# Performance work log

Measured on AMD Instinct MI355X. Metric: run time of the kernel, lower is better.

## Reference

```python
import jax, jax.numpy as jnp
import numpy as np

B, L, N, D = 32, 48, 325, 128


def setup_inputs() -> dict:
    key = jax.random.key(0)
    k1, k2, k3, k4, k5 = jax.random.split(key, 5)
    s = 1.0 / np.sqrt(D)  # PyTorch GRUCell init scale
    return {
        "X": jax.random.normal(k1, (B, L, N, D), dtype=jnp.float32),
        "W_ih": jax.random.uniform(k2, (3 * D, D), jnp.float32, -s, s),
        "W_hh": jax.random.uniform(k3, (3 * D, D), jnp.float32, -s, s),
        "b_ih": jax.random.uniform(k4, (3 * D,), jnp.float32, -s, s),
        "b_hh": jax.random.uniform(k5, (3 * D,), jnp.float32, -s, s),
    }


def reference(X, W_ih, W_hh, b_ih, b_hh):
    # X: (B, L, N, D) -> (B*N, L, D), matching X.transpose(1,2).reshape(B*N, L, D)
    b, l, n, d = X.shape
    x = jnp.transpose(X, (0, 2, 1, 3)).reshape(b * n, l, d)
    # Precompute all input-side gate projections once: (BN, L, 3D)
    gi = jnp.einsum("tlf,gf->tlg", x, W_ih) + b_ih
    gi_t = jnp.swapaxes(gi, 0, 1)  # (L, BN, 3D) for scan over time

    def step(h, gi_step):
        gh = h @ W_hh.T + b_hh  # (BN, 3D)
        i_r, i_z, i_n = jnp.split(gi_step, 3, axis=-1)
        h_r, h_z, h_n = jnp.split(gh, 3, axis=-1)
        r = jax.nn.sigmoid(i_r + h_r)
        z = jax.nn.sigmoid(i_z + h_z)
        ng = jnp.tanh(i_n + r * h_n)
        h_new = (1.0 - z) * ng + z * h
        return h_new, h_new

    h0 = jnp.zeros((b * n, d), dtype=X.dtype)
    _, outs = jax.lax.scan(step, h0, gi_t)
    # Dropout is identity in eval mode; original stacks along dim 0 -> (L, B*N, D)
    return outs
```

## Files before the change

kernel.cpp:

```cpp
#include <hip/hip_runtime.h>
#include <hip/hip_bf16.h>
#include <stdint.h>


constexpr int Bdim = 32;
constexpr int Ldim = 48;
constexpr int Nseq = 325;
constexpr int Ddim = 128;
constexpr int BN   = Bdim * Nseq;
constexpr int MT   = 48;
constexpr int NBLK = (BN + MT - 1) / MT;
constexpr int RS   = 136;
constexpr int XR32 = 528;
constexpr int XR16 = 272;
constexpr int HBUF_B = 2 * MT * RS * 2;
constexpr int SMEM_B = HBUF_B + 2 * MT * XR32;

typedef __bf16 bf16;
typedef __bf16 bf16x4 __attribute__((ext_vector_type(4)));
typedef __bf16 bf16x8 __attribute__((ext_vector_type(8)));
typedef float  floatx4 __attribute__((ext_vector_type(4)));
typedef float  floatx8 __attribute__((ext_vector_type(8)));

__device__ __forceinline__ float fast_sigmoid(float x) {
    return __builtin_amdgcn_rcpf(1.f + __expf(-x));
}
__device__ __forceinline__ float fast_tanh(float x) {
    const float e = __expf(-2.f * __builtin_fabsf(x));
    const float t = (1.f - e) * __builtin_amdgcn_rcpf(1.f + e);
    return __builtin_copysignf(t, x);
}

__device__ __forceinline__ bool detect_f32(const void* wih) {
    const bf16* p = (const bf16*)wih;
    bool f32 = false;
#pragma unroll
    for (int i = 0; i < 128; i += 2) {
        const float v = __builtin_fabsf((float)p[i]);
        if (!(v <= 0.125f)) f32 = true;
    }
    return f32;
}

template <bool F32>
__device__ __forceinline__ bf16x8 load8(const void* base, size_t off) {
    if constexpr (F32) {
        const floatx8 v = *(const floatx8*)((const float*)base + off);
        return __builtin_convertvector(v, bf16x8);
    } else {
        return *(const bf16x8*)((const bf16*)base + off);
    }
}
template <bool F32>
__device__ __forceinline__ float lds1(const void* base, int i) {
    if constexpr (F32) return ((const float*)base)[i];
    else               return (float)((const bf16*)base)[i];
}

__device__ __forceinline__ void gload_lds4(const void* g, void* l) {
    __builtin_amdgcn_global_load_lds(
        (const __attribute__((address_space(1))) void*)g,
        (__attribute__((address_space(3))) void*)l, 4, 0, 0);
}

template <bool F32>
__device__ __forceinline__ bf16x8 xfrag(const char* xb, int row, int kbase) {
    if constexpr (F32) {
        const float* p = (const float*)(xb + row * XR32) + kbase;
        const floatx4 a = *(const floatx4*)p;
        const floatx4 b = *(const floatx4*)(p + 4);
        const bf16x4 lo = __builtin_convertvector(a, bf16x4);
        const bf16x4 hi = __builtin_convertvector(b, bf16x4);
        return __builtin_shufflevector(lo, hi, 0, 1, 2, 3, 4, 5, 6, 7);
    } else {
        return *(const bf16x8*)((const bf16*)(xb + row * XR16) + kbase);
    }
}

template <bool F32>
__device__ __forceinline__ void gru_body(
    const void* __restrict__ X, const void* __restrict__ Wih,
    const void* __restrict__ Whh, const void* __restrict__ bih,
    const void* __restrict__ bhh, void* __restrict__ out,
    char* __restrict__ smem)
{
    const int tid  = threadIdx.x;
    const int wave = tid >> 6;
    const int lane = tid & 63;
    const int l16  = lane & 15;
    const int q    = lane >> 4;
    const int t0   = blockIdx.x * MT;
    const int dcol = wave * 16 + l16;

    bf16* hbuf = (bf16*)smem;
    char* xbuf = smem + HBUF_B;
    constexpr int XROWB   = F32 ? XR32 : XR16;
    constexpr int XBUF_B  = MT * XROWB;
    constexpr uint32_t lstride = (uint32_t)Nseq * Ddim * (F32 ? 4u : 2u);

    bf16x8 wih_f[3][4], whh_f[3][4];
#pragma unroll
    for (int g = 0; g < 3; ++g) {
        const size_t rowoffw = (size_t)(g * 128 + dcol) * Ddim + q * 8;
#pragma unroll
        for (int kk = 0; kk < 4; ++kk) {
            wih_f[g][kk] = load8<F32>(Wih, rowoffw + kk * 32);
            whh_f[g][kk] = load8<F32>(Whh, rowoffw + kk * 32);
        }
    }

    const float bias_r  = lds1<F32>(bih, dcol)       + lds1<F32>(bhh, dcol);
    const float bias_z  = lds1<F32>(bih, 128 + dcol) + lds1<F32>(bhh, 128 + dcol);
    const float bias_in = lds1<F32>(bih, 256 + dcol);
    const float bias_hn = lds1<F32>(bhh, 256 + dcol);

    const int srow0 = wave * 6;
    const char* Xc = (const char*)X;
    uint32_t rowoff[6];
#pragma unroll
    for (int i = 0; i < 6; ++i) {
        int t = t0 + srow0 + i;
        if (t >= BN) t = BN - 1;
        const int b = t / Nseq;
        const int n = t - b * Nseq;
        rowoff[i] = (((uint32_t)b * (Ldim * Nseq) + (uint32_t)n) * Ddim) * (F32 ? 4u : 2u)
                  + ((uint32_t)lane << 2);
    }

    auto stage = [&](char* xb, uint32_t loff) {
#pragma unroll
        for (int i = 0; i < 6; ++i) {
            const char* g = Xc + rowoff[i] + loff;
            char* d = xb + (srow0 + i) * XROWB;
            gload_lds4(g, d);
            if constexpr (F32) gload_lds4(g + 256, d + 256);
        }
    };

    for (int i = tid; i < MT * RS; i += 512) hbuf[i] = (bf16)0.f;
    stage(xbuf, 0);
    floatx4 hreg[3];
#pragma unroll
    for (int mt = 0; mt < 3; ++mt) hreg[mt] = floatx4{0.f, 0.f, 0.f, 0.f};
    __syncthreads();

    int cur = 0;
    for (int l = 0; l < Ldim; ++l) {
        const char* xc = xbuf + cur * XBUF_B;
        const bf16* hc = hbuf + cur * (MT * RS);

        bf16x8 xf[3][4];
#pragma unroll
        for (int mt = 0; mt < 3; ++mt)
#pragma unroll
            for (int kk = 0; kk < 4; ++kk)
                xf[mt][kk] = xfrag<F32>(xc, mt * 16 + l16, kk * 32 + q * 8);

        if (l + 1 < Ldim) stage(xbuf + (cur ^ 1) * XBUF_B, (uint32_t)(l + 1) * lstride);

        floatx4 acc_r[3], acc_z[3], acc_in[3], acc_hn[3];
#pragma unroll
        for (int mt = 0; mt < 3; ++mt) {
            acc_r[mt]  = floatx4{bias_r,  bias_r,  bias_r,  bias_r};
            acc_z[mt]  = floatx4{bias_z,  bias_z,  bias_z,  bias_z};
            acc_in[mt] = floatx4{bias_in, bias_in, bias_in, bias_in};
            acc_hn[mt] = floatx4{bias_hn, bias_hn, bias_hn, bias_hn};
        }

#pragma unroll
        for (int kk = 0; kk < 4; ++kk) {
#pragma unroll
            for (int mt = 0; mt < 3; ++mt) {
                const bf16x8 af = *(const bf16x8*)&hc[(mt * 16 + l16) * RS + kk * 32 + q * 8];
                acc_r[mt]  = __builtin_amdgcn_mfma_f32_16x16x32_bf16(af, whh_f[0][kk], acc_r[mt],  0, 0, 0);
                acc_z[mt]  = __builtin_amdgcn_mfma_f32_16x16x32_bf16(af, whh_f[1][kk], acc_z[mt],  0, 0, 0);
                acc_hn[mt] = __builtin_amdgcn_mfma_f32_16x16x32_bf16(af, whh_f[2][kk], acc_hn[mt], 0, 0, 0);
            }
        }
#pragma unroll
        for (int kk = 0; kk < 4; ++kk) {
#pragma unroll
            for (int mt = 0; mt < 3; ++mt) {
                acc_r[mt]  = __builtin_amdgcn_mfma_f32_16x16x32_bf16(xf[mt][kk], wih_f[0][kk], acc_r[mt],  0, 0, 0);
                acc_z[mt]  = __builtin_amdgcn_mfma_f32_16x16x32_bf16(xf[mt][kk], wih_f[1][kk], acc_z[mt],  0, 0, 0);
                acc_in[mt] = __builtin_amdgcn_mfma_f32_16x16x32_bf16(xf[mt][kk], wih_f[2][kk], acc_in[mt], 0, 0, 0);
            }
        }

        const int nxt = cur ^ 1;
        bf16* hn = hbuf + nxt * (MT * RS);
#pragma unroll
        for (int mt = 0; mt < 3; ++mt) {
            floatx4 hnew;
#pragma unroll
            for (int r = 0; r < 4; ++r) {
                const float rg = fast_sigmoid(acc_r[mt][r]);
                const float zg = fast_sigmoid(acc_z[mt][r]);
                const float ng = fast_tanh(acc_in[mt][r] + rg * acc_hn[mt][r]);
                const float h  = (1.f - zg) * ng + zg * hreg[mt][r];
                hnew[r] = h;
                const int m = mt * 16 + q * 4 + r;
                hn[m * RS + dcol] = (bf16)h;
                const int t = t0 + m;
                if (t < BN) {
                    const size_t oi = ((size_t)l * BN + t) * Ddim + dcol;
                    if constexpr (F32) ((float*)out)[oi] = h;
                    else               ((bf16*)out)[oi]  = (bf16)h;
                }
            }
            hreg[mt] = hnew;
        }
        __syncthreads();
        cur = nxt;
    }
}

__global__ __launch_bounds__(512, 2) void gru_rnn_kernel(
    const void* __restrict__ X, const void* __restrict__ Wih,
    const void* __restrict__ Whh, const void* __restrict__ bih,
    const void* __restrict__ bhh, void* __restrict__ out)
{
    __shared__ __align__(16) char smem[SMEM_B];
    if (detect_f32(Wih)) gru_body<true >(X, Wih, Whh, bih, bhh, out, smem);
    else                 gru_body<false>(X, Wih, Whh, bih, bhh, out, smem);
}

extern "C" void kernel_launch(void* const* d_in, const int* in_sizes, int n_in,
                              void* d_out, int out_size, void* d_ws, size_t ws_size,
                              hipStream_t stream) {
    hipLaunchKernelGGL(gru_rnn_kernel, dim3(NBLK), dim3(512), 0, stream,
                       d_in[0], d_in[1], d_in[2], d_in[3], d_in[4], d_out);
}
```

Measured before the change: 507.2 us.

## Stage X through registers as bf16 and use LDS-only barrier per step

Replaces the direct global-to-LDS async loads of X with register loads issued early in the step and written to LDS as bf16 after the gate math. This halves the LDS footprint for fp32 input and removes per-fragment conversion in the inner loop. The full __syncthreads is replaced by a barrier that only waits on LDS counters, so outstanding global stores are not waited on each step. Output addresses and masks are precomputed, and the h update is algebraically simplified. A redundant load is issued on the last step, and holding the prefetched X in registers raises register pressure.

```diff
diff --git a/kernel.cpp b/kernel.cpp
--- a/kernel.cpp
+++ b/kernel.cpp
@@ -11,14 +11,15 @@
 constexpr int MT   = 48;
 constexpr int NBLK = (BN + MT - 1) / MT;
 constexpr int RS   = 136;
-constexpr int XR32 = 528;
-constexpr int XR16 = 272;
+constexpr int XR   = 272;
 constexpr int HBUF_B = 2 * MT * RS * 2;
-constexpr int SMEM_B = HBUF_B + 2 * MT * XR32;
+constexpr int XBUF_B = MT * XR;
+constexpr int SMEM_B = HBUF_B + 2 * XBUF_B;
 
 typedef __bf16 bf16;
-typedef __bf16 bf16x4 __attribute__((ext_vector_type(4)));
+typedef __bf16 bf16x2 __attribute__((ext_vector_type(2)));
 typedef __bf16 bf16x8 __attribute__((ext_vector_type(8)));
+typedef float  floatx2 __attribute__((ext_vector_type(2)));
 typedef float  floatx4 __attribute__((ext_vector_type(4)));
 typedef float  floatx8 __attribute__((ext_vector_type(8)));
 
@@ -29,6 +30,14 @@
     const float e = __expf(-2.f * __builtin_fabsf(x));
     const float t = (1.f - e) * __builtin_amdgcn_rcpf(1.f + e);
     return __builtin_copysignf(t, x);
+}
+
+__device__ __forceinline__ void sync_lds_only() {
+    __builtin_amdgcn_sched_barrier(0);
+    asm volatile("s_waitcnt lgkmcnt(0)" ::: "memory");
+    __builtin_amdgcn_sched_barrier(0);
+    __builtin_amdgcn_s_barrier();
+    __builtin_amdgcn_sched_barrier(0);
 }
 
 __device__ __forceinline__ bool detect_f32(const void* wih) {
@@ -55,26 +64,6 @@
 __device__ __forceinline__ float lds1(const void* base, int i) {
     if constexpr (F32) return ((const float*)base)[i];
     else               return (float)((const bf16*)base)[i];
-}
-
-__device__ __forceinline__ void gload_lds4(const void* g, void* l) {
-    __builtin_amdgcn_global_load_lds(
-        (const __attribute__((address_space(1))) void*)g,
-        (__attribute__((address_space(3))) void*)l, 4, 0, 0);
-}
-
-template <bool F32>
-__device__ __forceinline__ bf16x8 xfrag(const char* xb, int row, int kbase) {
-    if constexpr (F32) {
-        const float* p = (const float*)(xb + row * XR32) + kbase;
-        const floatx4 a = *(const floatx4*)p;
-        const floatx4 b = *(const floatx4*)(p + 4);
-        const bf16x4 lo = __builtin_convertvector(a, bf16x4);
-        const bf16x4 hi = __builtin_convertvector(b, bf16x4);
-        return __builtin_shufflevector(lo, hi, 0, 1, 2, 3, 4, 5, 6, 7);
-    } else {
-        return *(const bf16x8*)((const bf16*)(xb + row * XR16) + kbase);
-    }
 }
 
 template <bool F32>
@@ -94,9 +83,6 @@
 
     bf16* hbuf = (bf16*)smem;
     char* xbuf = smem + HBUF_B;
-    constexpr int XROWB   = F32 ? XR32 : XR16;
-    constexpr int XBUF_B  = MT * XROWB;
-    constexpr uint32_t lstride = (uint32_t)Nseq * Ddim * (F32 ? 4u : 2u);
 
     bf16x8 wih_f[3][4], whh_f[3][4];
 #pragma unroll
@@ -114,8 +100,9 @@
     const float bias_in = lds1<F32>(bih, 256 + dcol);
     const float bias_hn = lds1<F32>(bhh, 256 + dcol);
 
-    const int srow0 = wave * 6;
-    const char* Xc = (const char*)X;
+    const int   srow0 = wave * 6;
+    const char* Xc    = (const char*)X;
+    const uint32_t lstride = (uint32_t)(Nseq * Ddim) * (F32 ? 4u : 2u);
     uint32_t rowoff[6];
 #pragma unroll
     for (int i = 0; i < 6; ++i) {
@@ -123,22 +110,50 @@
         if (t >= BN) t = BN - 1;
         const int b = t / Nseq;
         const int n = t - b * Nseq;
-        rowoff[i] = (((uint32_t)b * (Ldim * Nseq) + (uint32_t)n) * Ddim) * (F32 ? 4u : 2u)
-                  + ((uint32_t)lane << 2);
-    }
-
-    auto stage = [&](char* xb, uint32_t loff) {
+        rowoff[i] = (uint32_t)(b * (Ldim * Nseq) + n) * Ddim * (F32 ? 4u : 2u)
+                  + ((uint32_t)lane << (F32 ? 3 : 2));
+    }
+
+    floatx2  vf[6];
+    uint32_t vb[6];
+    auto stage_load = [&](int l) {
+        const char* Xl = Xc + (uint32_t)l * lstride;
 #pragma unroll
         for (int i = 0; i < 6; ++i) {
-            const char* g = Xc + rowoff[i] + loff;
-            char* d = xb + (srow0 + i) * XROWB;
-            gload_lds4(g, d);
-            if constexpr (F32) gload_lds4(g + 256, d + 256);
+            if constexpr (F32) vf[i] = *(const floatx2*)(Xl + rowoff[i]);
+            else               vb[i] = *(const uint32_t*)(Xl + rowoff[i]);
         }
     };
+    auto stage_write = [&](char* xb) {
+#pragma unroll
+        for (int i = 0; i < 6; ++i) {
+            uint32_t w;
+            if constexpr (F32) {
+                union { bf16x2 h; uint32_t u; } cv;
+                cv.h = __builtin_convertvector(vf[i], bf16x2);
+                w = cv.u;
+            } else {
+                w = vb[i];
+            }
+            *(uint32_t*)(xb + (srow0 + i) * XR + (lane << 2)) = w;
+        }
+    };
+
+    constexpr size_t esz = F32 ? 4 : 2;
+    const size_t OSTEP = (size_t)BN * Ddim * esz;
+    size_t obyte[3];
+    bool   msk[3][4];
+#pragma unroll
+    for (int mt = 0; mt < 3; ++mt) {
+        const int trow = t0 + mt * 16 + q * 4;
+        obyte[mt] = ((size_t)trow * Ddim + dcol) * esz;
+#pragma unroll
+        for (int r = 0; r < 4; ++r) msk[mt][r] = (trow + r) < BN;
+    }
 
     for (int i = tid; i < MT * RS; i += 512) hbuf[i] = (bf16)0.f;
-    stage(xbuf, 0);
+    stage_load(0);
+    stage_write(xbuf);
     floatx4 hreg[3];
 #pragma unroll
     for (int mt = 0; mt < 3; ++mt) hreg[mt] = floatx4{0.f, 0.f, 0.f, 0.f};
@@ -154,9 +169,10 @@
         for (int mt = 0; mt < 3; ++mt)
 #pragma unroll
             for (int kk = 0; kk < 4; ++kk)
-                xf[mt][kk] = xfrag<F32>(xc, mt * 16 + l16, kk * 32 + q * 8);
-
-        if (l + 1 < Ldim) stage(xbuf + (cur ^ 1) * XBUF_B, (uint32_t)(l + 1) * lstride);
+                xf[mt][kk] = *(const bf16x8*)(xc + (mt * 16 + l16) * XR + kk * 64 + q * 16);
+
+        const int lp = (l + 1 < Ldim) ? (l + 1) : (Ldim - 1);
+        stage_load(lp);
 
         floatx4 acc_r[3], acc_z[3], acc_in[3], acc_hn[3];
 #pragma unroll
@@ -197,20 +213,22 @@
                 const float rg = fast_sigmoid(acc_r[mt][r]);
                 const float zg = fast_sigmoid(acc_z[mt][r]);
                 const float ng = fast_tanh(acc_in[mt][r] + rg * acc_hn[mt][r]);
-                const float h  = (1.f - zg) * ng + zg * hreg[mt][r];
+                const float h  = ng + zg * (hreg[mt][r] - ng);
                 hnew[r] = h;
-                const int m = mt * 16 + q * 4 + r;
-                hn[m * RS + dcol] = (bf16)h;
-                const int t = t0 + m;
-                if (t < BN) {
-                    const size_t oi = ((size_t)l * BN + t) * Ddim + dcol;
-                    if constexpr (F32) ((float*)out)[oi] = h;
-                    else               ((bf16*)out)[oi]  = (bf16)h;
+                hn[(mt * 16 + q * 4 + r) * RS + dcol] = (bf16)h;
+                if (msk[mt][r]) {
+                    char* op = (char*)out + obyte[mt] + (size_t)(r * Ddim) * esz;
+                    if constexpr (F32) *(float*)op = h;
+                    else               *(bf16*)op  = (bf16)h;
                 }
             }
-            hreg[mt] = hnew;
-        }
-        __syncthreads();
+            hreg[mt]  = hnew;
+            obyte[mt] += OSTEP;
+        }
+
+        stage_write(xbuf + nxt * XBUF_B);
+
+        sync_lds_only();
         cur = nxt;
     }
 }
```

Result: faster. 454.7 us (-10.3%).
